# Optimization experiments

Hardware: AMD Instinct MI355X
Metric: run time of the kernel (lower is better)

Reference implementation:

```python
import jax, jax.numpy as jnp
import numpy as np

B, M, R = 2, 2048, 256
H, DH = 16, 64
ROPE_THETA = 10000.0


def setup_inputs() -> dict:
    key = jax.random.key(0)
    ks = jax.random.split(key, 9)
    d = H * DH
    inp = {
        "Pq": jax.random.normal(ks[0], (B, M, R), jnp.float32),
        "Pk": jax.random.normal(ks[1], (B, M, R), jnp.float32),
        "Pv": jax.random.normal(ks[2], (B, M, R), jnp.float32),
        "Vq": jax.random.normal(ks[3], (R, d), jnp.float32) / np.sqrt(R),
        "Vk": jax.random.normal(ks[4], (R, d), jnp.float32) / np.sqrt(R),
        "Vv": jax.random.normal(ks[5], (R, d), jnp.float32) / np.sqrt(R),
        "bq": jax.random.normal(ks[6], (d,), jnp.float32),
        "bk": jax.random.normal(ks[7], (d,), jnp.float32),
        "bv": jax.random.normal(ks[8], (d,), jnp.float32),
        "attention_mask": jnp.ones((B, M), jnp.int32),
        "position_ids": jnp.tile(jnp.arange(M, dtype=jnp.int32), (B, 1)),
    }
    return inp


def _rope_cos_sin(position_ids):
    # half-half RoPE tables; kernel only reads the first half of cos/sin
    inv_freq = 1.0 / (ROPE_THETA ** (jnp.arange(0, DH, 2, dtype=jnp.float32) / DH))
    freqs = position_ids.astype(jnp.float32)[:, :, None] * inv_freq[None, None, :]  # [B,M,DH/2]
    return jnp.cos(freqs)[:, None], jnp.sin(freqs)[:, None]  # [B,1,M,DH/2]


def _heads(P, V, b):
    # low-rank reconstruction: [B,M,R] @ [R,H*DH] + [H*DH] -> [B,H,M,DH]
    x = jnp.einsum('bmr,rd->bmd', P, V) + b
    return x.reshape(x.shape[0], x.shape[1], H, DH).transpose(0, 2, 1, 3)


def _rotate(x, cos, sin):
    x0, x1 = x[..., :DH // 2], x[..., DH // 2:]
    return jnp.concatenate([x0 * cos - x1 * sin, x0 * sin + x1 * cos], axis=-1)


def reference(Pq, Pk, Pv, Vq, Vk, Vv, bq, bk, bv, attention_mask, position_ids):
    cos, sin = _rope_cos_sin(position_ids)
    q = _rotate(_heads(Pq, Vq, bq), cos, sin)  # [B,H,M,DH]
    k = _rotate(_heads(Pk, Vk, bk), cos, sin)
    v = _heads(Pv, Vv, bv)
    scale = 1.0 / jnp.sqrt(jnp.float32(DH))
    scores = jnp.einsum('bhmd,bhnd->bhmn', q, k) * scale
    keep = attention_mask.astype(bool)[:, None, None, :]
    scores = jnp.where(keep, scores, -jnp.inf)
    # online-softmax equivalent with all-masked-row zeroing (matches kernel)
    mx = jnp.max(scores, axis=-1, keepdims=True)
    safe_mx = jnp.where(jnp.isfinite(mx), mx, 0.0)
    p = jnp.exp(scores - safe_mx)
    l = jnp.sum(p, axis=-1, keepdims=True)
    out = jnp.einsum('bhmn,bhnd->bhmd', p, v) / jnp.where(l > 0, l, 1.0)
    out = jnp.where(l > 0, out, 0.0)
    return out  # [B,H,M,DH]
```

## Files before the change

kernel.cpp:

```cpp
#include <hip/hip_runtime.h>
#include <cstdint>
#include <cstddef>

#define Bc 2
#define Mc 2048
#define Rc 256
#define Hc 16
#define DHc 64
#define Dc (Hc * DHc)
#define NKT2 16

typedef __attribute__((ext_vector_type(8))) short short8;
typedef __attribute__((ext_vector_type(4))) float float4v;
typedef __attribute__((ext_vector_type(4))) unsigned short ushort4v;
typedef __attribute__((ext_vector_type(8))) unsigned short ushort8v;
typedef __attribute__((ext_vector_type(4))) unsigned int uint4v;

#if __has_builtin(__builtin_amdgcn_exp2f)
#define EXPFN(x) __builtin_amdgcn_exp2f(x)
#define QSCALE 0.18033688f
#define MADD_KEEP (-28.8539008f)
#else
#define EXPFN(x) __expf(x)
#define QSCALE 0.125f
#define MADD_KEEP (-20.0f)
#endif

__device__ inline unsigned short f2bf(float f) {
    union { float f; uint32_t u; } v;
    v.f = f;
    uint32_t r = v.u + 0x7fffu + ((v.u >> 16) & 1u);
    return (unsigned short)(r >> 16);
}

__device__ inline int swz(int row, int chunk) {
    return row * 128 + ((chunk ^ (row & 7)) << 4);
}

__global__ __launch_bounds__(256)
void transpose_v(const float* __restrict__ V0, const float* __restrict__ V1,
                 const float* __restrict__ V2, unsigned short* __restrict__ Vt)
{
    const int mat = blockIdx.z;
    const float* src = mat == 0 ? V0 : (mat == 1 ? V1 : V2);
    const int d  = blockIdx.x * 256 + threadIdx.x;
    const int kg = blockIdx.y;
    short8 v;
    #pragma unroll
    for (int j = 0; j < 8; ++j)
        v[j] = (short)f2bf(src[(size_t)(kg * 8 + j) * Dc + d]);
    *(short8*)&Vt[((size_t)mat * Dc + d) * Rc + kg * 8] = v;
}

__global__ __launch_bounds__(256)
void proj_kernel(const float* __restrict__ Pq, const float* __restrict__ Pk,
                 const float* __restrict__ Pv,
                 const unsigned short* __restrict__ Vtp,
                 const float* __restrict__ bq, const float* __restrict__ bk,
                 const float* __restrict__ bv,
                 const int* __restrict__ pos_ids,
                 unsigned short* __restrict__ Qb, unsigned short* __restrict__ Kb,
                 unsigned short* __restrict__ Vta)
{
    __shared__ __align__(16) unsigned char AtB[128 * 128];
    __shared__ __align__(16) unsigned char BtB[128 * 128];

    const int tid = threadIdx.x;
    const int z = blockIdx.z, mat = z >> 1, b = z & 1;
    const int m0 = blockIdx.x * 128, d0 = blockIdx.y * 128;
    const int w = tid >> 6, lane = tid & 63, col = lane & 15, quad = lane >> 4;
    const int mh = w & 1, dh2 = w >> 1;

    const float* P = mat == 0 ? Pq : (mat == 1 ? Pk : Pv);
    const float* Pg = P + ((size_t)b * Mc + m0) * Rc;
    const unsigned short* Vg = Vtp + (size_t)mat * Dc * Rc + (size_t)d0 * Rc;

    const int arow = tid >> 1, ac0 = (tid & 1) * 4;
    const int brow = tid >> 1, bc0 = (tid & 1) * 4;

    float4v acc[4][4] = {};

    for (int kc = 0; kc < 4; ++kc) {
        float4 af[8];
        uint4v br[4];
        #pragma unroll
        for (int i = 0; i < 8; ++i)
            af[i] = *(const float4*)&Pg[(size_t)arow * Rc + kc * 64 + (tid & 1) * 32 + i * 4];
        #pragma unroll
        for (int i = 0; i < 4; ++i)
            br[i] = *(const uint4v*)&Vg[(size_t)brow * Rc + kc * 64 + (bc0 + i) * 8];
        ushort8v ua[4];
        #pragma unroll
        for (int i = 0; i < 4; ++i) {
            float4 f0 = af[2 * i], f1 = af[2 * i + 1];
            ushort8v u = { f2bf(f0.x), f2bf(f0.y), f2bf(f0.z), f2bf(f0.w),
                           f2bf(f1.x), f2bf(f1.y), f2bf(f1.z), f2bf(f1.w) };
            ua[i] = u;
        }
        __syncthreads();
        #pragma unroll
        for (int i = 0; i < 4; ++i) {
            *(ushort8v*)(AtB + swz(arow, ac0 + i)) = ua[i];
            *(uint4v*)(BtB + swz(brow, bc0 + i)) = br[i];
        }
        __syncthreads();

        #pragma unroll
        for (int kk = 0; kk < 2; ++kk) {
            short8 afr[4], bfr[4];
            #pragma unroll
            for (int mt = 0; mt < 4; ++mt)
                afr[mt] = *(const short8*)(AtB + swz(mh * 64 + mt * 16 + col, kk * 4 + quad));
            #pragma unroll
            for (int dt = 0; dt < 4; ++dt)
                bfr[dt] = *(const short8*)(BtB + swz(dh2 * 64 + dt * 16 + col, kk * 4 + quad));
            #pragma unroll
            for (int mt = 0; mt < 4; ++mt)
                #pragma unroll
                for (int dt = 0; dt < 4; ++dt)
                    acc[mt][dt] = __builtin_amdgcn_mfma_f32_16x16x32_bf16(
                        afr[mt], bfr[dt], acc[mt][dt], 0, 0, 0);
        }
    }

    const int head = (d0 + dh2 * 64) >> 6;
    const int bh = b * Hc + head;

    if (mat < 2) {
        const float* bias = mat == 0 ? bq : bk;
        unsigned short* outp = mat == 0 ? Qb : Kb;
        const float oscale = mat == 0 ? QSCALE : 1.0f;
        float b00 = bias[head * 64 + col],      b01 = bias[head * 64 + 16 + col];
        float b10 = bias[head * 64 + 32 + col], b11 = bias[head * 64 + 48 + col];
        float if0 = __expf(-0.28782314f * (float)col);
        float if1 = __expf(-0.28782314f * (float)(col + 16));
        #pragma unroll
        for (int mt = 0; mt < 4; ++mt)
            #pragma unroll
            for (int r = 0; r < 4; ++r) {
                int m = m0 + mh * 64 + mt * 16 + quad * 4 + r;
                float pos = (float)pos_ids[b * Mc + m];
                float a0 = pos * if0, a1 = pos * if1;
                float cs0 = __cosf(a0), sn0 = __sinf(a0);
                float cs1 = __cosf(a1), sn1 = __sinf(a1);
                float x00 = acc[mt][0][r] + b00, x10 = acc[mt][2][r] + b10;
                float x01 = acc[mt][1][r] + b01, x11 = acc[mt][3][r] + b11;
                unsigned short* og = outp + ((size_t)bh * Mc + m) * DHc;
                og[col]      = f2bf((x00 * cs0 - x10 * sn0) * oscale);
                og[32 + col] = f2bf((x00 * sn0 + x10 * cs0) * oscale);
                og[16 + col] = f2bf((x01 * cs1 - x11 * sn1) * oscale);
                og[48 + col] = f2bf((x01 * sn1 + x11 * cs1) * oscale);
            }
    } else {
        #pragma unroll
        for (int dt = 0; dt < 4; ++dt) {
            int d = d0 + dh2 * 64 + dt * 16 + col;
            float bb = bv[d];
            int dh = d & 63;
            #pragma unroll
            for (int mt = 0; mt < 4; ++mt) {
                ushort4v pv;
                #pragma unroll
                for (int r = 0; r < 4; ++r) pv[r] = f2bf(acc[mt][dt][r] + bb);
                size_t base = ((size_t)bh * DHc + dh) * Mc + m0 + mh * 64 + mt * 16 + quad * 4;
                *(ushort4v*)&Vta[base] = pv;
            }
        }
    }
}

__global__ __launch_bounds__(256, 2)
void attn_kernel(const unsigned short* __restrict__ Qb,
                 const unsigned short* __restrict__ Kb,
                 const unsigned short* __restrict__ Vt,
                 const int* __restrict__ mask,
                 float* __restrict__ out)
{
    __shared__ __align__(16) unsigned char smem[65536];

    const int tid = threadIdx.x;
    const int q0 = blockIdx.x * 128;
    const int bh = blockIdx.y;
    const int b  = bh >> 4;
    const int w = tid >> 6, lane = tid & 63, col = lane & 15, quad = lane >> 4;
    const int s = w >> 1, qh = w & 1;

    unsigned char* KsB = smem + s * 8192;
    unsigned char* VsB = smem + 16384 + s * 8192;
    unsigned char* PsB = smem + 32768 + w * 8192;

    short8 qf[4][2];
    #pragma unroll
    for (int qg = 0; qg < 4; ++qg) {
        const unsigned short* Qg =
            Qb + ((size_t)bh * Mc + q0 + qh * 64 + qg * 16 + col) * DHc + quad * 8;
        qf[qg][0] = *(const short8*)Qg;
        qf[qg][1] = *(const short8*)(Qg + 32);
    }

    const int ts = tid & 127;
    const int srow = ts >> 1, sc0 = (ts & 1) * 4;
    const unsigned short* Kg = Kb + ((size_t)bh * Mc + s * (Mc / 2)) * DHc;
    const unsigned short* Vg = Vt + (size_t)bh * DHc * Mc + s * (Mc / 2);
    const int* mp = mask + b * Mc + s * (Mc / 2);

    uint4v kr[4], vr[4];
    #pragma unroll
    for (int i = 0; i < 4; ++i) {
        kr[i] = *(const uint4v*)&Kg[(size_t)srow * DHc + (sc0 + i) * 8];
        vr[i] = *(const uint4v*)&Vg[(size_t)srow * Mc + (sc0 + i) * 8];
    }

    float lsum[4] = {};
    float4v acc_o[4][4] = {};

    for (int kt = 0; kt < NKT2; ++kt) {
        __syncthreads();
        #pragma unroll
        for (int i = 0; i < 4; ++i) {
            *(uint4v*)(KsB + swz(srow, sc0 + i)) = kr[i];
            *(uint4v*)(VsB + swz(srow, sc0 + i)) = vr[i];
        }
        __syncthreads();

        if (kt + 1 < NKT2) {
            const unsigned short* Kn = Kg + (size_t)(kt + 1) * 64 * DHc;
            #pragma unroll
            for (int i = 0; i < 4; ++i) {
                kr[i] = *(const uint4v*)&Kn[(size_t)srow * DHc + (sc0 + i) * 8];
                vr[i] = *(const uint4v*)&Vg[(size_t)srow * Mc + (kt + 1) * 64 + (sc0 + i) * 8];
            }
        }

        #pragma unroll
        for (int ks = 0; ks < 4; ++ks) {
            int4 mv = *(const int4*)&mp[kt * 64 + ks * 16 + quad * 4];
            const int* mi = (const int*)&mv;
            float md[4];
            #pragma unroll
            for (int r = 0; r < 4; ++r) md[r] = mi[r] ? MADD_KEEP : -1e30f;
            short8 a0 = *(const short8*)(KsB + swz(ks * 16 + col, quad));
            short8 a1 = *(const short8*)(KsB + swz(ks * 16 + col, 4 + quad));
            #pragma unroll
            for (int qg = 0; qg < 4; ++qg) {
                float4v sacc = {};
                sacc = __builtin_amdgcn_mfma_f32_16x16x32_bf16(a0, qf[qg][0], sacc, 0, 0, 0);
                sacc = __builtin_amdgcn_mfma_f32_16x16x32_bf16(a1, qf[qg][1], sacc, 0, 0, 0);
                ushort4v pw;
                #pragma unroll
                for (int r = 0; r < 4; ++r) {
                    float p = EXPFN(sacc[r] + md[r]);
                    lsum[qg] += p;
                    union { float f; uint32_t u; } cv; cv.f = p;
                    pw[r] = (unsigned short)((cv.u + 0x8000u) >> 16);
                }
                int qrow = qg * 16 + col;
                *(ushort4v*)(PsB + qrow * 128 +
                             (((ks * 2 + (quad >> 1)) ^ (qrow & 7)) << 4) +
                             (quad & 1) * 8) = pw;
            }
        }

        #pragma unroll
        for (int kk = 0; kk < 2; ++kk) {
            short8 pa[4];
            #pragma unroll
            for (int qg = 0; qg < 4; ++qg)
                pa[qg] = *(const short8*)(PsB + swz(qg * 16 + col, kk * 4 + quad));
            #pragma unroll
            for (int dh = 0; dh < 4; ++dh) {
                short8 vb = *(const short8*)(VsB + swz(dh * 16 + col, kk * 4 + quad));
                #pragma unroll
                for (int qg = 0; qg < 4; ++qg)
                    acc_o[qg][dh] = __builtin_amdgcn_mfma_f32_16x16x32_bf16(
                        pa[qg], vb, acc_o[qg][dh], 0, 0, 0);
            }
        }
    }

    #pragma unroll
    for (int qg = 0; qg < 4; ++qg) {
        lsum[qg] += __shfl_xor(lsum[qg], 16);
        lsum[qg] += __shfl_xor(lsum[qg], 32);
    }

    __syncthreads();
    float* Of = (float*)(smem + 32768 + qh * 16384);
    float* Lf = (float*)smem;
    if (s == 1) {
        #pragma unroll
        for (int qg = 0; qg < 4; ++qg)
            #pragma unroll
            for (int dh = 0; dh < 4; ++dh)
                #pragma unroll
                for (int r = 0; r < 4; ++r)
                    Of[(qg * 16 + quad * 4 + r) * 64 + dh * 16 + col] = acc_o[qg][dh][r];
        if (quad == 0) {
            #pragma unroll
            for (int qg = 0; qg < 4; ++qg)
                Lf[qh * 64 + qg * 16 + col] = lsum[qg];
        }
    }
    __syncthreads();
    if (s == 0) {
        #pragma unroll
        for (int qg = 0; qg < 4; ++qg)
            #pragma unroll
            for (int r = 0; r < 4; ++r) {
                float l0 = __shfl(lsum[qg], quad * 4 + r);
                float l1 = Lf[qh * 64 + qg * 16 + quad * 4 + r];
                float lt = l0 + l1;
                float inv = (lt > 0.0f) ? 1.0f / lt : 0.0f;
                int m = q0 + qh * 64 + qg * 16 + quad * 4 + r;
                float* og = out + ((size_t)bh * Mc + m) * DHc;
                #pragma unroll
                for (int dh = 0; dh < 4; ++dh)
                    og[dh * 16 + col] =
                        (acc_o[qg][dh][r] + Of[(qg * 16 + quad * 4 + r) * 64 + dh * 16 + col]) * inv;
            }
    }
}

extern "C" void kernel_launch(void* const* d_in, const int* in_sizes, int n_in,
                              void* d_out, int out_size, void* d_ws, size_t ws_size,
                              hipStream_t stream) {
    const float* Pq = (const float*)d_in[0];
    const float* Pk = (const float*)d_in[1];
    const float* Pv = (const float*)d_in[2];
    const float* Vq = (const float*)d_in[3];
    const float* Vk = (const float*)d_in[4];
    const float* Vv = (const float*)d_in[5];
    const float* bq = (const float*)d_in[6];
    const float* bk = (const float*)d_in[7];
    const float* bv = (const float*)d_in[8];
    const int*   am = (const int*)d_in[9];
    const int*   pid = (const int*)d_in[10];
    float* out = (float*)d_out;

    const size_t n_el = (size_t)Bc * Hc * Mc * DHc;
    unsigned short* Qb  = (unsigned short*)d_ws;
    unsigned short* Kb  = Qb + n_el;
    unsigned short* Vta = Kb + n_el;
    unsigned short* Vtp = Vta + n_el;

    dim3 blk(256);
    transpose_v<<<dim3(Dc / 256, Rc / 8, 3), blk, 0, stream>>>(Vq, Vk, Vv, Vtp);

    proj_kernel<<<dim3(Mc / 128, Dc / 128, 6), blk, 0, stream>>>(
        Pq, Pk, Pv, Vtp, bq, bk, bv, pid, Qb, Kb, Vta);

    attn_kernel<<<dim3(Mc / 128, Bc * Hc), blk, 0, stream>>>(Qb, Kb, Vta, am, out);
}
```

Measured before the change: 175.5 us.

## Load K/V fragments directly from global per wave, drop shared K/V staging and split-K merge

The attention kernel no longer stages K and V tiles in shared memory with block-wide barriers, and no longer splits the key range across two wave pairs that are merged at the end. Each of the four waves now owns 32 query rows, walks all key tiles, and loads its K and V MFMA operand fragments straight from global memory, so only the per-wave P buffer stays in LDS. This removes the __syncthreads pairs, the LDS traffic and the cross-wave reduction. In exchange, every wave re-reads the full K/V from global or cache with no register prefetch across iterations. Probability rounding now uses the HIP bf16 conversion intrinsics.

Result: slower. 240.2 us (+36.9%).

```diff
diff --git a/kernel.cpp b/kernel.cpp
--- a/kernel.cpp
+++ b/kernel.cpp
@@ -1,4 +1,5 @@
 #include <hip/hip_runtime.h>
+#include <hip/hip_bf16.h>
 #include <cstdint>
 #include <cstddef>
 
@@ -8,7 +9,7 @@
 #define Hc 16
 #define DHc 64
 #define Dc (Hc * DHc)
-#define NKT2 16
+#define NKT (Mc / 64)
 
 typedef __attribute__((ext_vector_type(8))) short short8;
 typedef __attribute__((ext_vector_type(4))) float float4v;
@@ -176,149 +177,118 @@
                  const int* __restrict__ mask,
                  float* __restrict__ out)
 {
-    __shared__ __align__(16) unsigned char smem[65536];
+    __shared__ __align__(16) unsigned char PsAll[4][4096];
 
     const int tid = threadIdx.x;
     const int q0 = blockIdx.x * 128;
     const int bh = blockIdx.y;
     const int b  = bh >> 4;
     const int w = tid >> 6, lane = tid & 63, col = lane & 15, quad = lane >> 4;
-    const int s = w >> 1, qh = w & 1;
-
-    unsigned char* KsB = smem + s * 8192;
-    unsigned char* VsB = smem + 16384 + s * 8192;
-    unsigned char* PsB = smem + 32768 + w * 8192;
-
-    short8 qf[4][2];
-    #pragma unroll
-    for (int qg = 0; qg < 4; ++qg) {
+    unsigned char* PsB = PsAll[w];
+
+    short8 qf[2][2];
+    #pragma unroll
+    for (int qs = 0; qs < 2; ++qs) {
         const unsigned short* Qg =
-            Qb + ((size_t)bh * Mc + q0 + qh * 64 + qg * 16 + col) * DHc + quad * 8;
-        qf[qg][0] = *(const short8*)Qg;
-        qf[qg][1] = *(const short8*)(Qg + 32);
-    }
-
-    const int ts = tid & 127;
-    const int srow = ts >> 1, sc0 = (ts & 1) * 4;
-    const unsigned short* Kg = Kb + ((size_t)bh * Mc + s * (Mc / 2)) * DHc;
-    const unsigned short* Vg = Vt + (size_t)bh * DHc * Mc + s * (Mc / 2);
-    const int* mp = mask + b * Mc + s * (Mc / 2);
-
-    uint4v kr[4], vr[4];
-    #pragma unroll
-    for (int i = 0; i < 4; ++i) {
-        kr[i] = *(const uint4v*)&Kg[(size_t)srow * DHc + (sc0 + i) * 8];
-        vr[i] = *(const uint4v*)&Vg[(size_t)srow * Mc + (sc0 + i) * 8];
-    }
-
-    float lsum[4] = {};
-    float4v acc_o[4][4] = {};
-
-    for (int kt = 0; kt < NKT2; ++kt) {
-        __syncthreads();
-        #pragma unroll
-        for (int i = 0; i < 4; ++i) {
-            *(uint4v*)(KsB + swz(srow, sc0 + i)) = kr[i];
-            *(uint4v*)(VsB + swz(srow, sc0 + i)) = vr[i];
-        }
-        __syncthreads();
-
-        if (kt + 1 < NKT2) {
-            const unsigned short* Kn = Kg + (size_t)(kt + 1) * 64 * DHc;
-            #pragma unroll
-            for (int i = 0; i < 4; ++i) {
-                kr[i] = *(const uint4v*)&Kn[(size_t)srow * DHc + (sc0 + i) * 8];
-                vr[i] = *(const uint4v*)&Vg[(size_t)srow * Mc + (kt + 1) * 64 + (sc0 + i) * 8];
+            Qb + ((size_t)bh * Mc + q0 + w * 32 + qs * 16 + col) * DHc + quad * 8;
+        qf[qs][0] = *(const short8*)Qg;
+        qf[qs][1] = *(const short8*)(Qg + 32);
+    }
+
+    const unsigned short* kp = Kb + ((size_t)bh * Mc + col) * DHc + quad * 8;
+    const unsigned short* vp[4];
+    #pragma unroll
+    for (int ds = 0; ds < 4; ++ds)
+        vp[ds] = Vt + ((size_t)bh * DHc + ds * 16 + col) * Mc + quad * 8;
+    const int* mp = mask + b * Mc + quad * 4;
+
+    float lsum[2] = {};
+    float4v acc_o[2][4] = {};
+
+    for (int kt = 0; kt < NKT; ++kt) {
+        short8 ka0[4], ka1[4];
+        #pragma unroll
+        for (int ks = 0; ks < 4; ++ks) {
+            const unsigned short* ra = kp + (size_t)(kt * 64 + ks * 16) * DHc;
+            ka0[ks] = *(const short8*)ra;
+            ka1[ks] = *(const short8*)(ra + 32);
+        }
+        short8 vb[4][2];
+        #pragma unroll
+        for (int ds = 0; ds < 4; ++ds)
+            #pragma unroll
+            for (int kk = 0; kk < 2; ++kk)
+                vb[ds][kk] = *(const short8*)(vp[ds] + kt * 64 + kk * 32);
+        int4 mv[4];
+        #pragma unroll
+        for (int ks = 0; ks < 4; ++ks)
+            mv[ks] = *(const int4*)(mp + kt * 64 + ks * 16);
+
+        float4v sacc[4][2] = {};
+        #pragma unroll
+        for (int ks = 0; ks < 4; ++ks)
+            #pragma unroll
+            for (int qs = 0; qs < 2; ++qs) {
+                sacc[ks][qs] = __builtin_amdgcn_mfma_f32_16x16x32_bf16(
+                    ka0[ks], qf[qs][0], sacc[ks][qs], 0, 0, 0);
+                sacc[ks][qs] = __builtin_amdgcn_mfma_f32_16x16x32_bf16(
+                    ka1[ks], qf[qs][1], sacc[ks][qs], 0, 0, 0);
             }
-        }
 
         #pragma unroll
         for (int ks = 0; ks < 4; ++ks) {
-            int4 mv = *(const int4*)&mp[kt * 64 + ks * 16 + quad * 4];
-            const int* mi = (const int*)&mv;
-            float md[4];
-            #pragma unroll
-            for (int r = 0; r < 4; ++r) md[r] = mi[r] ? MADD_KEEP : -1e30f;
-            short8 a0 = *(const short8*)(KsB + swz(ks * 16 + col, quad));
-            short8 a1 = *(const short8*)(KsB + swz(ks * 16 + col, 4 + quad));
-            #pragma unroll
-            for (int qg = 0; qg < 4; ++qg) {
-                float4v sacc = {};
-                sacc = __builtin_amdgcn_mfma_f32_16x16x32_bf16(a0, qf[qg][0], sacc, 0, 0, 0);
-                sacc = __builtin_amdgcn_mfma_f32_16x16x32_bf16(a1, qf[qg][1], sacc, 0, 0, 0);
-                ushort4v pw;
-                #pragma unroll
-                for (int r = 0; r < 4; ++r) {
-                    float p = EXPFN(sacc[r] + md[r]);
-                    lsum[qg] += p;
-                    union { float f; uint32_t u; } cv; cv.f = p;
-                    pw[r] = (unsigned short)((cv.u + 0x8000u) >> 16);
-                }
-                int qrow = qg * 16 + col;
+            const int* mi = (const int*)&mv[ks];
+            #pragma unroll
+            for (int qs = 0; qs < 2; ++qs) {
+                float p0 = EXPFN(sacc[ks][qs][0] + (mi[0] ? MADD_KEEP : -1e30f));
+                float p1 = EXPFN(sacc[ks][qs][1] + (mi[1] ? MADD_KEEP : -1e30f));
+                float p2 = EXPFN(sacc[ks][qs][2] + (mi[2] ? MADD_KEEP : -1e30f));
+                float p3 = EXPFN(sacc[ks][qs][3] + (mi[3] ? MADD_KEEP : -1e30f));
+                lsum[qs] += (p0 + p1) + (p2 + p3);
+                __hip_bfloat162 h01 = __float22bfloat162_rn(float2{p0, p1});
+                __hip_bfloat162 h23 = __float22bfloat162_rn(float2{p2, p3});
+                union { struct { __hip_bfloat162 a, b; } h; ushort4v u; } cv;
+                cv.h.a = h01; cv.h.b = h23;
+                int qrow = qs * 16 + col;
                 *(ushort4v*)(PsB + qrow * 128 +
                              (((ks * 2 + (quad >> 1)) ^ (qrow & 7)) << 4) +
-                             (quad & 1) * 8) = pw;
+                             (quad & 1) * 8) = cv.u;
             }
         }
 
         #pragma unroll
         for (int kk = 0; kk < 2; ++kk) {
-            short8 pa[4];
-            #pragma unroll
-            for (int qg = 0; qg < 4; ++qg)
-                pa[qg] = *(const short8*)(PsB + swz(qg * 16 + col, kk * 4 + quad));
-            #pragma unroll
-            for (int dh = 0; dh < 4; ++dh) {
-                short8 vb = *(const short8*)(VsB + swz(dh * 16 + col, kk * 4 + quad));
+            short8 pa[2];
+            #pragma unroll
+            for (int qs = 0; qs < 2; ++qs)
+                pa[qs] = *(const short8*)(PsB + swz(qs * 16 + col, kk * 4 + quad));
+            #pragma unroll
+            for (int ds = 0; ds < 4; ++ds)
                 #pragma unroll
-                for (int qg = 0; qg < 4; ++qg)
-                    acc_o[qg][dh] = __builtin_amdgcn_mfma_f32_16x16x32_bf16(
-                        pa[qg], vb, acc_o[qg][dh], 0, 0, 0);
-            }
-        }
-    }
-
-    #pragma unroll
-    for (int qg = 0; qg < 4; ++qg) {
-        lsum[qg] += __shfl_xor(lsum[qg], 16);
-        lsum[qg] += __shfl_xor(lsum[qg], 32);
-    }
-
-    __syncthreads();
-    float* Of = (float*)(smem + 32768 + qh * 16384);
-    float* Lf = (float*)smem;
-    if (s == 1) {
-        #pragma unroll
-        for (int qg = 0; qg < 4; ++qg)
-            #pragma unroll
-            for (int dh = 0; dh < 4; ++dh)
-                #pragma unroll
-                for (int r = 0; r < 4; ++r)
-                    Of[(qg * 16 + quad * 4 + r) * 64 + dh * 16 + col] = acc_o[qg][dh][r];
-        if (quad == 0) {
-            #pragma unroll
-            for (int qg = 0; qg < 4; ++qg)
-                Lf[qh * 64 + qg * 16 + col] = lsum[qg];
-        }
-    }
-    __syncthreads();
-    if (s == 0) {
-        #pragma unroll
-        for (int qg = 0; qg < 4; ++qg)
-            #pragma unroll
-            for (int r = 0; r < 4; ++r) {
-                float l0 = __shfl(lsum[qg], quad * 4 + r);
-                float l1 = Lf[qh * 64 + qg * 16 + quad * 4 + r];
-                float lt = l0 + l1;
-                float inv = (lt > 0.0f) ? 1.0f / lt : 0.0f;
-                int m = q0 + qh * 64 + qg * 16 + quad * 4 + r;
-                float* og = out + ((size_t)bh * Mc + m) * DHc;
-                #pragma unroll
-                for (int dh = 0; dh < 4; ++dh)
-                    og[dh * 16 + col] =
-                        (acc_o[qg][dh][r] + Of[(qg * 16 + quad * 4 + r) * 64 + dh * 16 + col]) * inv;
-            }
-    }
+                for (int qs = 0; qs < 2; ++qs)
+                    acc_o[qs][ds] = __builtin_amdgcn_mfma_f32_16x16x32_bf16(
+                        pa[qs], vb[ds][kk], acc_o[qs][ds], 0, 0, 0);
+        }
+    }
+
+    #pragma unroll
+    for (int qs = 0; qs < 2; ++qs) {
+        lsum[qs] += __shfl_xor(lsum[qs], 16);
+        lsum[qs] += __shfl_xor(lsum[qs], 32);
+    }
+
+    #pragma unroll
+    for (int qs = 0; qs < 2; ++qs)
+        #pragma unroll
+        for (int r = 0; r < 4; ++r) {
+            float lr = __shfl(lsum[qs], quad * 4 + r);
+            float inv = (lr > 0.0f) ? 1.0f / lr : 0.0f;
+            int m = q0 + w * 32 + qs * 16 + quad * 4 + r;
+            float* og = out + ((size_t)bh * Mc + m) * DHc;
+            #pragma unroll
+            for (int ds = 0; ds < 4; ++ds)
+                og[ds * 16 + col] = acc_o[qs][ds][r] * inv;
+        }
 }
 
 extern "C" void kernel_launch(void* const* d_in, const int* in_sizes, int n_in,
```
